# Kernel tuning notes

Measured on AMD Instinct MI355X. Metric: run time of the kernel, lower is better.

## Reference

```python
import jax, jax.numpy as jnp
import numpy as np

H = 1024
V = 50257
L = 512


def setup_inputs() -> dict:
    key = jax.random.key(0)
    ks = jax.random.split(key, 12)
    s = 0.02
    return {
        "input_tok": jax.random.randint(ks[0], (1,), 0, V, dtype=jnp.int64),
        "hidden": jax.random.normal(ks[1], (1, 1, H), dtype=jnp.float32),
        "encoder_outputs": jax.random.normal(ks[2], (L, 1, H), dtype=jnp.float32),
        "embedding_w": jax.random.normal(ks[3], (V, H), dtype=jnp.float32) * s,
        "attn_combine_w": jax.random.normal(ks[4], (H, 2 * H), dtype=jnp.float32) * s,
        "attn_combine_b": jax.random.normal(ks[5], (H,), dtype=jnp.float32) * s,
        "w_ih": jax.random.normal(ks[6], (3 * H, H), dtype=jnp.float32) * s,
        "w_hh": jax.random.normal(ks[7], (3 * H, H), dtype=jnp.float32) * s,
        "b_ih": jax.random.normal(ks[8], (3 * H,), dtype=jnp.float32) * s,
        "b_hh": jax.random.normal(ks[9], (3 * H,), dtype=jnp.float32) * s,
        "out_w": jax.random.normal(ks[10], (V, H), dtype=jnp.float32) * s,
        "out_b": jax.random.normal(ks[11], (V,), dtype=jnp.float32) * s,
    }


def reference(input_tok, hidden, encoder_outputs, embedding_w,
              attn_combine_w, attn_combine_b, w_ih, w_hh, b_ih, b_hh,
              out_w, out_b):
    # embedding(input).view(1,1,-1); dropout is identity in eval mode
    embedded = embedding_w[input_tok[0]][None, :]          # [1, H]
    enc = encoder_outputs[:, 0, :]                          # [L, H]
    h0 = hidden[0]                                          # [1, H]
    # dot-product attention: hidden[0] @ enc^T
    attn_weights = jax.nn.softmax(h0 @ enc.T, axis=1)      # [1, L]
    attn_applied = attn_weights @ enc                       # [1, H]
    combined = jnp.concatenate([embedded, attn_applied], axis=1)  # [1, 2H]
    x = jax.nn.relu(combined @ attn_combine_w.T + attn_combine_b)  # [1, H]
    # single-step GRU cell (PyTorch gate ordering: r, z, n)
    gi = x @ w_ih.T + b_ih                                  # [1, 3H]
    gh = h0 @ w_hh.T + b_hh                                 # [1, 3H]
    r = jax.nn.sigmoid(gi[:, :H] + gh[:, :H])
    z = jax.nn.sigmoid(gi[:, H:2 * H] + gh[:, H:2 * H])
    n = jnp.tanh(gi[:, 2 * H:] + r * gh[:, 2 * H:])
    h_new = (1.0 - z) * n + z * h0                          # [1, H]
    logp = jax.nn.log_softmax(h_new @ out_w.T + out_b, axis=1)  # [1, V]
    return logp, h_new[None], attn_weights
```

## Files before the change

kernel.cpp:

```cpp
#include <hip/hip_runtime.h>
#include <math.h>

#define H  1024
#define H2 2048
#define H3 3072
#define V  50257
#define L  512

__device__ __forceinline__ float dot4(float4 a, float4 b) {
    return a.x*b.x + a.y*b.y + a.z*b.z + a.w*b.w;
}
__device__ __forceinline__ float wave_red_sum(float acc) {
    for (int off = 32; off > 0; off >>= 1) acc += __shfl_down(acc, off, 64);
    return acc;
}

__global__ void __launch_bounds__(256) k_pre(
        const float* __restrict__ h0, const float* __restrict__ enc,
        const float* __restrict__ w_hh, const float* __restrict__ b_hh,
        float* __restrict__ scores, float* __restrict__ gh) {
    __shared__ float s[4];
    int t = threadIdx.x, lane = t & 63, wv = t >> 6;
    if (blockIdx.x < 512) {
        int l = blockIdx.x;
        float4 a = ((const float4*)(enc + (size_t)l * H))[t];
        float4 b = ((const float4*)h0)[t];
        float acc = wave_red_sum(dot4(a, b));
        if (lane == 0) s[wv] = acc;
        __syncthreads();
        if (t == 0) scores[l] = s[0] + s[1] + s[2] + s[3];
    } else {
        int row = (blockIdx.x - 512) * 4 + wv;
        const float4* wr = (const float4*)(w_hh + (size_t)row * H);
        const float4* h4 = (const float4*)h0;
        float acc = 0.f;
        #pragma unroll
        for (int j = 0; j < 4; ++j) acc += dot4(wr[j * 64 + lane], h4[j * 64 + lane]);
        acc = wave_red_sum(acc);
        if (lane == 0) gh[row] = acc + b_hh[row];
    }
}

__global__ void __launch_bounds__(256) k_softmax_attn(
        const float* __restrict__ enc, const float* __restrict__ scores,
        float* __restrict__ attn_applied, float* __restrict__ d_out) {
    __shared__ float wl[L];
    __shared__ float red[256];
    __shared__ float part[8][32];
    int t = threadIdx.x;
    float s0 = scores[t], s1 = scores[t + 256];
    red[t] = fmaxf(s0, s1);
    __syncthreads();
    for (int off = 128; off > 0; off >>= 1) {
        if (t < off) red[t] = fmaxf(red[t], red[t + off]);
        __syncthreads();
    }
    float gmax = red[0];
    __syncthreads();
    float e0 = expf(s0 - gmax), e1 = expf(s1 - gmax);
    red[t] = e0 + e1;
    __syncthreads();
    for (int off = 128; off > 0; off >>= 1) {
        if (t < off) red[t] += red[t + off];
        __syncthreads();
    }
    float inv = 1.0f / red[0];
    wl[t]       = e0 * inv;
    wl[t + 256] = e1 * inv;
    __syncthreads();
    if (blockIdx.x == 0) {
        d_out[V + H + t]       = wl[t];
        d_out[V + H + t + 256] = wl[t + 256];
    }
    int c = t & 31, sIdx = t >> 5;
    int col = blockIdx.x * 32 + c;
    float acc = 0.f;
    for (int l = sIdx * 64; l < sIdx * 64 + 64; ++l)
        acc += wl[l] * enc[(size_t)l * H + col];
    part[sIdx][c] = acc;
    __syncthreads();
    if (sIdx == 0) {
        float sum = 0.f;
        #pragma unroll
        for (int k = 0; k < 8; ++k) sum += part[k][c];
        attn_applied[col] = sum;
    }
}

__global__ void __launch_bounds__(256) k_combine(
        const float* __restrict__ emb_w, const int* __restrict__ tok,
        const float* __restrict__ attn_applied, const float* __restrict__ Wc,
        const float* __restrict__ bc, float* __restrict__ x) {
    __shared__ float comb[H2];
    int t = threadIdx.x;
    int tk = tok[0];
    ((float4*)comb)[t]       = ((const float4*)(emb_w + (size_t)tk * H))[t];
    ((float4*)comb)[t + 256] = ((const float4*)attn_applied)[t];
    __syncthreads();
    int lane = t & 63, wv = t >> 6;
    int row = blockIdx.x * 4 + wv;
    const float4* wr = (const float4*)(Wc + (size_t)row * H2);
    float acc = 0.f;
    #pragma unroll
    for (int j = 0; j < 8; ++j) acc += dot4(wr[j * 64 + lane], ((const float4*)comb)[j * 64 + lane]);
    acc = wave_red_sum(acc);
    if (lane == 0) x[row] = fmaxf(acc + bc[row], 0.f);
}

__global__ void __launch_bounds__(256) k_gi_gru(
        const float* __restrict__ x, const float* __restrict__ h0,
        const float* __restrict__ w_ih, const float* __restrict__ b_ih,
        const float* __restrict__ gh, float* __restrict__ d_out,
        float* __restrict__ hnew) {
    int t = threadIdx.x, lane = t & 63, wv = t >> 6;
    int i = blockIdx.x * 4 + wv;
    const float4* xv = (const float4*)x;
    float g[3];
    #pragma unroll
    for (int k = 0; k < 3; ++k) {
        const float4* wr = (const float4*)(w_ih + (size_t)(k * H + i) * H);
        float acc = 0.f;
        #pragma unroll
        for (int j = 0; j < 4; ++j) acc += dot4(wr[j * 64 + lane], xv[j * 64 + lane]);
        g[k] = wave_red_sum(acc);
    }
    if (lane == 0) {
        float gir = g[0] + b_ih[i];
        float giz = g[1] + b_ih[H + i];
        float gin = g[2] + b_ih[2 * H + i];
        float r = 1.f / (1.f + expf(-(gir + gh[i])));
        float z = 1.f / (1.f + expf(-(giz + gh[H + i])));
        float n = tanhf(gin + r * gh[2 * H + i]);
        float h = (1.f - z) * n + z * h0[i];
        d_out[V + i] = h;
        hnew[i] = h;
    }
}

__global__ void __launch_bounds__(256) k_logits(
        const float* __restrict__ hnew, const float* __restrict__ out_w,
        const float* __restrict__ out_b, float* __restrict__ logits) {
    __shared__ float hs[H];
    int t = threadIdx.x;
    ((float4*)hs)[t] = ((const float4*)hnew)[t];
    __syncthreads();
    int lane = t & 63, wv = t >> 6;
    int row0 = (blockIdx.x * 4 + wv) * 2;
    if (row0 >= V) return;
    const float4* hs4 = (const float4*)hs;
    const float4* w0 = (const float4*)(out_w + (size_t)row0 * H);
    float acc0 = 0.f, acc1 = 0.f;
    if (row0 + 1 < V) {
        const float4* w1 = (const float4*)(out_w + (size_t)(row0 + 1) * H);
        #pragma unroll
        for (int j = 0; j < 4; ++j) {
            float4 b = hs4[j * 64 + lane];
            acc0 += dot4(w0[j * 64 + lane], b);
            acc1 += dot4(w1[j * 64 + lane], b);
        }
        for (int off = 32; off > 0; off >>= 1) {
            acc0 += __shfl_down(acc0, off, 64);
            acc1 += __shfl_down(acc1, off, 64);
        }
        if (lane == 0) {
            logits[row0]     = acc0 + out_b[row0];
            logits[row0 + 1] = acc1 + out_b[row0 + 1];
        }
    } else {
        #pragma unroll
        for (int j = 0; j < 4; ++j) acc0 += dot4(w0[j * 64 + lane], hs4[j * 64 + lane]);
        acc0 = wave_red_sum(acc0);
        if (lane == 0) logits[row0] = acc0 + out_b[row0];
    }
}

__global__ void __launch_bounds__(256) k_lse_part(
        const float* __restrict__ logits, float* __restrict__ pm,
        float* __restrict__ ps) {
    __shared__ float red[4];
    int b = blockIdx.x, t = threadIdx.x, lane = t & 63, wv = t >> 6;
    const int CH = (V + 63) / 64;
    int begin = b * CH;
    int end = begin + CH; if (end > V) end = V;
    float v[4]; int cnt = 0;
    for (int i = begin + t; i < end; i += 256) v[cnt++] = logits[i];
    float m = -INFINITY;
    for (int c = 0; c < cnt; ++c) m = fmaxf(m, v[c]);
    for (int off = 32; off > 0; off >>= 1) m = fmaxf(m, __shfl_down(m, off, 64));
    if (lane == 0) red[wv] = m;
    __syncthreads();
    float M = fmaxf(fmaxf(red[0], red[1]), fmaxf(red[2], red[3]));
    __syncthreads();
    float s = 0.f;
    for (int c = 0; c < cnt; ++c) s += expf(v[c] - M);
    s = wave_red_sum(s);
    if (lane == 0) red[wv] = s;
    __syncthreads();
    if (t == 0) {
        pm[b] = M;
        ps[b] = red[0] + red[1] + red[2] + red[3];
    }
}

__global__ void __launch_bounds__(256) k_logp(
        float* __restrict__ d_out, const float* __restrict__ pm,
        const float* __restrict__ ps) {
    __shared__ float sh[2];
    int t = threadIdx.x;
    if (t < 64) {
        float m = pm[t], s = ps[t];
        float M = m;
        for (int off = 32; off > 0; off >>= 1) M = fmaxf(M, __shfl_down(M, off, 64));
        M = __shfl(M, 0, 64);
        float sc = s * expf(m - M);
        sc = wave_red_sum(sc);
        if (t == 0) { sh[0] = M; sh[1] = logf(sc); }
    }
    __syncthreads();
    float M = sh[0], Ls = sh[1];
    int i = blockIdx.x * 256 + t;
    if (i < V) d_out[i] = d_out[i] - M - Ls;
}

extern "C" void kernel_launch(void* const* d_in, const int* in_sizes, int n_in,
                              void* d_out, int out_size, void* d_ws, size_t ws_size,
                              hipStream_t stream) {
    const int*   tok    = (const int*)d_in[0];
    const float* hidden = (const float*)d_in[1];
    const float* enc    = (const float*)d_in[2];
    const float* emb_w  = (const float*)d_in[3];
    const float* Wc     = (const float*)d_in[4];
    const float* bc     = (const float*)d_in[5];
    const float* w_ih   = (const float*)d_in[6];
    const float* w_hh   = (const float*)d_in[7];
    const float* b_ih   = (const float*)d_in[8];
    const float* b_hh   = (const float*)d_in[9];
    const float* out_w  = (const float*)d_in[10];
    const float* out_b  = (const float*)d_in[11];
    float* out = (float*)d_out;
    float* ws  = (float*)d_ws;

    float* scores       = ws;
    float* gh           = ws + 1024;
    float* attn_applied = ws + 4096;
    float* xbuf         = ws + 5120;
    float* hnew         = ws + 6144;
    float* pm           = ws + 7168;
    float* psum         = ws + 7232;

    k_pre         <<<1280, 256, 0, stream>>>(hidden, enc, w_hh, b_hh, scores, gh);
    k_softmax_attn<<<32,   256, 0, stream>>>(enc, scores, attn_applied, out);
    k_combine     <<<256,  256, 0, stream>>>(emb_w, tok, attn_applied, Wc, bc, xbuf);
    k_gi_gru      <<<256,  256, 0, stream>>>(xbuf, hidden, w_ih, b_ih, gh, out, hnew);
    k_logits      <<<(V + 7) / 8, 256, 0, stream>>>(hnew, out_w, out_b, out);
    k_lse_part    <<<64,   256, 0, stream>>>(out, pm, psum);
    k_logp        <<<(V + 255) / 256, 256, 0, stream>>>(out, pm, psum);
}
```

Measured before the change: 417.0 us.

## Fuse log-sum-exp partials into logits kernel with last-block reduction

The logits kernel now computes four rows per wave instead of two, and each block writes its local max and sum-exp partials. The last block to finish, detected through an atomic counter, reduces all partials into a global max and log-sum. This removes the separate LSE-partial kernel, its re-read of the logits, and one launch. The attention-score part of k_pre now does one row per wave, so it needs fewer blocks. The counter is reset inside k_pre, and the fused kernel adds a threadfence and atomic per block.

```diff
diff --git a/kernel.cpp b/kernel.cpp
--- a/kernel.cpp
+++ b/kernel.cpp
@@ -3,9 +3,9 @@
 
 #define H  1024
 #define H2 2048
-#define H3 3072
 #define V  50257
 #define L  512
+#define NBL ((V + 15) / 16)
 
 __device__ __forceinline__ float dot4(float4 a, float4 b) {
     return a.x*b.x + a.y*b.y + a.z*b.z + a.w*b.w;
@@ -18,21 +18,22 @@
 __global__ void __launch_bounds__(256) k_pre(
         const float* __restrict__ h0, const float* __restrict__ enc,
         const float* __restrict__ w_hh, const float* __restrict__ b_hh,
-        float* __restrict__ scores, float* __restrict__ gh) {
-    __shared__ float s[4];
+        float* __restrict__ scores, float* __restrict__ gh,
+        int* __restrict__ counter) {
     int t = threadIdx.x, lane = t & 63, wv = t >> 6;
-    if (blockIdx.x < 512) {
-        int l = blockIdx.x;
-        float4 a = ((const float4*)(enc + (size_t)l * H))[t];
-        float4 b = ((const float4*)h0)[t];
-        float acc = wave_red_sum(dot4(a, b));
-        if (lane == 0) s[wv] = acc;
-        __syncthreads();
-        if (t == 0) scores[l] = s[0] + s[1] + s[2] + s[3];
+    if (blockIdx.x == 0 && t == 0) counter[0] = 0;
+    const float4* h4 = (const float4*)h0;
+    if (blockIdx.x < 128) {
+        int l = blockIdx.x * 4 + wv;
+        const float4* e4 = (const float4*)(enc + (size_t)l * H);
+        float acc = 0.f;
+        #pragma unroll
+        for (int j = 0; j < 4; ++j) acc += dot4(e4[j * 64 + lane], h4[j * 64 + lane]);
+        acc = wave_red_sum(acc);
+        if (lane == 0) scores[l] = acc;
     } else {
-        int row = (blockIdx.x - 512) * 4 + wv;
+        int row = (blockIdx.x - 128) * 4 + wv;
         const float4* wr = (const float4*)(w_hh + (size_t)row * H);
-        const float4* h4 = (const float4*)h0;
         float acc = 0.f;
         #pragma unroll
         for (int j = 0; j < 4; ++j) acc += dot4(wr[j * 64 + lane], h4[j * 64 + lane]);
@@ -137,89 +138,94 @@
     }
 }
 
-__global__ void __launch_bounds__(256) k_logits(
+__global__ void __launch_bounds__(256) k_logits_lse(
         const float* __restrict__ hnew, const float* __restrict__ out_w,
-        const float* __restrict__ out_b, float* __restrict__ logits) {
+        const float* __restrict__ out_b, float* __restrict__ logits,
+        float* __restrict__ pm, float* __restrict__ ps,
+        int* __restrict__ counter, float* __restrict__ fin) {
     __shared__ float hs[H];
-    int t = threadIdx.x;
+    __shared__ float blk[16];
+    __shared__ float red[4];
+    __shared__ int last;
+    int t = threadIdx.x, lane = t & 63, wv = t >> 6;
     ((float4*)hs)[t] = ((const float4*)hnew)[t];
     __syncthreads();
-    int lane = t & 63, wv = t >> 6;
-    int row0 = (blockIdx.x * 4 + wv) * 2;
-    if (row0 >= V) return;
     const float4* hs4 = (const float4*)hs;
-    const float4* w0 = (const float4*)(out_w + (size_t)row0 * H);
-    float acc0 = 0.f, acc1 = 0.f;
-    if (row0 + 1 < V) {
-        const float4* w1 = (const float4*)(out_w + (size_t)(row0 + 1) * H);
-        #pragma unroll
-        for (int j = 0; j < 4; ++j) {
-            float4 b = hs4[j * 64 + lane];
-            acc0 += dot4(w0[j * 64 + lane], b);
-            acc1 += dot4(w1[j * 64 + lane], b);
+    int row0 = (blockIdx.x * 4 + wv) * 4;
+    int r0 = row0     < V ? row0     : V - 1;
+    int r1 = row0 + 1 < V ? row0 + 1 : V - 1;
+    int r2 = row0 + 2 < V ? row0 + 2 : V - 1;
+    int r3 = row0 + 3 < V ? row0 + 3 : V - 1;
+    const float4* w0 = (const float4*)(out_w + (size_t)r0 * H);
+    const float4* w1 = (const float4*)(out_w + (size_t)r1 * H);
+    const float4* w2 = (const float4*)(out_w + (size_t)r2 * H);
+    const float4* w3 = (const float4*)(out_w + (size_t)r3 * H);
+    float a0 = 0.f, a1 = 0.f, a2 = 0.f, a3 = 0.f;
+    #pragma unroll
+    for (int j = 0; j < 4; ++j) {
+        float4 b = hs4[j * 64 + lane];
+        a0 += dot4(w0[j * 64 + lane], b);
+        a1 += dot4(w1[j * 64 + lane], b);
+        a2 += dot4(w2[j * 64 + lane], b);
+        a3 += dot4(w3[j * 64 + lane], b);
+    }
+    for (int off = 32; off > 0; off >>= 1) {
+        a0 += __shfl_down(a0, off, 64);
+        a1 += __shfl_down(a1, off, 64);
+        a2 += __shfl_down(a2, off, 64);
+        a3 += __shfl_down(a3, off, 64);
+    }
+    if (lane == 0) {
+        float v0 = a0 + out_b[r0], v1 = a1 + out_b[r1];
+        float v2 = a2 + out_b[r2], v3 = a3 + out_b[r3];
+        if (row0     < V) logits[row0]     = v0; else v0 = -INFINITY;
+        if (row0 + 1 < V) logits[row0 + 1] = v1; else v1 = -INFINITY;
+        if (row0 + 2 < V) logits[row0 + 2] = v2; else v2 = -INFINITY;
+        if (row0 + 3 < V) logits[row0 + 3] = v3; else v3 = -INFINITY;
+        blk[wv * 4 + 0] = v0; blk[wv * 4 + 1] = v1;
+        blk[wv * 4 + 2] = v2; blk[wv * 4 + 3] = v3;
+    }
+    __syncthreads();
+    if (t == 0) {
+        float m = blk[0];
+        #pragma unroll
+        for (int k = 1; k < 16; ++k) m = fmaxf(m, blk[k]);
+        float s = 0.f;
+        #pragma unroll
+        for (int k = 0; k < 16; ++k) s += expf(blk[k] - m);
+        pm[blockIdx.x] = m;
+        ps[blockIdx.x] = s;
+        __threadfence();
+        int old = atomicAdd(counter, 1);
+        last = (old == (int)gridDim.x - 1) ? 1 : 0;
+    }
+    __syncthreads();
+    if (last) {
+        __threadfence();
+        float m = -INFINITY;
+        for (int i = t; i < NBL; i += 256) m = fmaxf(m, pm[i]);
+        for (int off = 32; off > 0; off >>= 1) m = fmaxf(m, __shfl_down(m, off, 64));
+        if (lane == 0) red[wv] = m;
+        __syncthreads();
+        float M = fmaxf(fmaxf(red[0], red[1]), fmaxf(red[2], red[3]));
+        __syncthreads();
+        float s = 0.f;
+        for (int i = t; i < NBL; i += 256) s += ps[i] * expf(pm[i] - M);
+        s = wave_red_sum(s);
+        if (lane == 0) red[wv] = s;
+        __syncthreads();
+        if (t == 0) {
+            fin[0] = M;
+            fin[1] = logf(red[0] + red[1] + red[2] + red[3]);
         }
-        for (int off = 32; off > 0; off >>= 1) {
-            acc0 += __shfl_down(acc0, off, 64);
-            acc1 += __shfl_down(acc1, off, 64);
-        }
-        if (lane == 0) {
-            logits[row0]     = acc0 + out_b[row0];
-            logits[row0 + 1] = acc1 + out_b[row0 + 1];
-        }
-    } else {
-        #pragma unroll
-        for (int j = 0; j < 4; ++j) acc0 += dot4(w0[j * 64 + lane], hs4[j * 64 + lane]);
-        acc0 = wave_red_sum(acc0);
-        if (lane == 0) logits[row0] = acc0 + out_b[row0];
-    }
-}
-
-__global__ void __launch_bounds__(256) k_lse_part(
-        const float* __restrict__ logits, float* __restrict__ pm,
-        float* __restrict__ ps) {
-    __shared__ float red[4];
-    int b = blockIdx.x, t = threadIdx.x, lane = t & 63, wv = t >> 6;
-    const int CH = (V + 63) / 64;
-    int begin = b * CH;
-    int end = begin + CH; if (end > V) end = V;
-    float v[4]; int cnt = 0;
-    for (int i = begin + t; i < end; i += 256) v[cnt++] = logits[i];
-    float m = -INFINITY;
-    for (int c = 0; c < cnt; ++c) m = fmaxf(m, v[c]);
-    for (int off = 32; off > 0; off >>= 1) m = fmaxf(m, __shfl_down(m, off, 64));
-    if (lane == 0) red[wv] = m;
-    __syncthreads();
-    float M = fmaxf(fmaxf(red[0], red[1]), fmaxf(red[2], red[3]));
-    __syncthreads();
-    float s = 0.f;
-    for (int c = 0; c < cnt; ++c) s += expf(v[c] - M);
-    s = wave_red_sum(s);
-    if (lane == 0) red[wv] = s;
-    __syncthreads();
-    if (t == 0) {
-        pm[b] = M;
-        ps[b] = red[0] + red[1] + red[2] + red[3];
     }
 }
 
 __global__ void __launch_bounds__(256) k_logp(
-        float* __restrict__ d_out, const float* __restrict__ pm,
-        const float* __restrict__ ps) {
-    __shared__ float sh[2];
-    int t = threadIdx.x;
-    if (t < 64) {
-        float m = pm[t], s = ps[t];
-        float M = m;
-        for (int off = 32; off > 0; off >>= 1) M = fmaxf(M, __shfl_down(M, off, 64));
-        M = __shfl(M, 0, 64);
-        float sc = s * expf(m - M);
-        sc = wave_red_sum(sc);
-        if (t == 0) { sh[0] = M; sh[1] = logf(sc); }
-    }
-    __syncthreads();
-    float M = sh[0], Ls = sh[1];
-    int i = blockIdx.x * 256 + t;
-    if (i < V) d_out[i] = d_out[i] - M - Ls;
+        float* __restrict__ d_out, const float* __restrict__ fin) {
+    int i = blockIdx.x * 256 + threadIdx.x;
+    float c = fin[0] + fin[1];
+    if (i < V) d_out[i] = d_out[i] - c;
 }
 
 extern "C" void kernel_launch(void* const* d_in, const int* in_sizes, int n_in,
@@ -246,13 +252,14 @@
     float* xbuf         = ws + 5120;
     float* hnew         = ws + 6144;
     float* pm           = ws + 7168;
-    float* psum         = ws + 7232;
-
-    k_pre         <<<1280, 256, 0, stream>>>(hidden, enc, w_hh, b_hh, scores, gh);
-    k_softmax_attn<<<32,   256, 0, stream>>>(enc, scores, attn_applied, out);
-    k_combine     <<<256,  256, 0, stream>>>(emb_w, tok, attn_applied, Wc, bc, xbuf);
-    k_gi_gru      <<<256,  256, 0, stream>>>(xbuf, hidden, w_ih, b_ih, gh, out, hnew);
-    k_logits      <<<(V + 7) / 8, 256, 0, stream>>>(hnew, out_w, out_b, out);
-    k_lse_part    <<<64,   256, 0, stream>>>(out, pm, psum);
-    k_logp        <<<(V + 255) / 256, 256, 0, stream>>>(out, pm, psum);
-}
+    float* psum         = ws + 10368;
+    int*   counter      = (int*)(ws + 13568);
+    float* fin          = ws + 13572;
+
+    k_pre         <<<896, 256, 0, stream>>>(hidden, enc, w_hh, b_hh, scores, gh, counter);
+    k_softmax_attn<<<32,  256, 0, stream>>>(enc, scores, attn_applied, out);
+    k_combine     <<<256, 256, 0, stream>>>(emb_w, tok, attn_applied, Wc, bc, xbuf);
+    k_gi_gru      <<<256, 256, 0, stream>>>(xbuf, hidden, w_ih, b_ih, gh, out, hnew);
+    k_logits_lse  <<<NBL, 256, 0, stream>>>(hnew, out_w, out_b, out, pm, psum, counter, fin);
+    k_logp        <<<(V + 255) / 256, 256, 0, stream>>>(out, fin);
+}
```

Measured after the change: 572.5 us. 37.3% more time.
